# Kernel tuning notes

Hardware: AMD Instinct MI355X
Metric: run time of the kernel (lower is better)

## Reference

```python
import jax, jax.numpy as jnp
import numpy as np

B, S, IN_D, OUT_D, QD = 4, 1024, 16, 16, 32
HID, HEADS, HD, L, TED = 256, 8, 32, 4, 256
DECAY = 0.1
SCALE = HD ** -0.5


def _ln(x):
    m = x.mean(-1, keepdims=True)
    v = ((x - m) ** 2).mean(-1, keepdims=True)
    return (x - m) * jax.lax.rsqrt(v + 1e-5)


def _lin(x, w, b):
    # torch nn.Linear: y = x @ W^T + b, W is [out, in]
    return jnp.einsum('...i,oi->...o', x, w) + b


def _sin_emb(t, dim):
    half = dim // 2
    freqs = jnp.exp(-np.log(10000.0) * jnp.arange(half, dtype=jnp.float32) / (half - 1))
    a = t[:, None] * freqs[None, :]
    return jnp.concatenate([jnp.sin(a), jnp.cos(a)], axis=-1)


def _mish(x):
    return x * jnp.tanh(jax.nn.softplus(x))


def _gelu(x):
    return jax.nn.gelu(x, approximate=False)


def setup_inputs() -> dict:
    key = jax.random.key(0)
    ks = iter(jax.random.split(key, 64))

    def w(shape):
        return jax.random.normal(next(ks), shape, dtype=jnp.float32) * 0.02

    d = {}
    d['x'] = jax.random.normal(next(ks), (B, S, IN_D), dtype=jnp.float32)
    d['query'] = jax.random.normal(next(ks), (B, QD), dtype=jnp.float32)
    d['time'] = jax.random.uniform(next(ks), (B,), dtype=jnp.float32) * 1000.0
    d['tm_w1'] = w((TED * 4, TED)); d['tm_b1'] = jnp.zeros((TED * 4,), jnp.float32)
    d['tm_w2'] = w((TED, TED * 4)); d['tm_b2'] = jnp.zeros((TED,), jnp.float32)
    d['in_w'] = w((HID, IN_D)); d['in_b'] = jnp.zeros((HID,), jnp.float32)
    d['q_w1'] = w((HID, QD)); d['q_b1'] = jnp.zeros((HID,), jnp.float32)
    d['q_w2'] = w((HID, HID)); d['q_b2'] = jnp.zeros((HID,), jnp.float32)
    d['n1_w'] = jnp.ones((L, HID), jnp.float32); d['n1_b'] = jnp.zeros((L, HID), jnp.float32)
    d['qkv_w'] = w((L, 3 * HID, HID)); d['qkv_b'] = jnp.zeros((L, 3 * HID), jnp.float32)
    d['ap_w'] = w((L, HID, HID)); d['ap_b'] = jnp.zeros((L, HID), jnp.float32)
    d['rel_bias'] = w((L, 2 * S - 1, HEADS))
    d['n2_w'] = jnp.ones((L, HID), jnp.float32); d['n2_b'] = jnp.zeros((L, HID), jnp.float32)
    d['f1_w'] = w((L, 4 * HID, HID)); d['f1_b'] = jnp.zeros((L, 4 * HID), jnp.float32)
    d['f2_w'] = w((L, HID, 4 * HID)); d['f2_b'] = jnp.zeros((L, HID), jnp.float32)
    d['t1_w'] = w((L, HID, TED)); d['t1_b'] = jnp.zeros((L, HID), jnp.float32)
    d['t2_w'] = w((L, HID, HID)); d['t2_b'] = jnp.zeros((L, HID), jnp.float32)
    d['out_w'] = w((OUT_D, HID)); d['out_b'] = jnp.zeros((OUT_D,), jnp.float32)
    return d


def reference(x, query, time, tm_w1, tm_b1, tm_w2, tm_b2, in_w, in_b,
              q_w1, q_b1, q_w2, q_b2, n1_w, n1_b, qkv_w, qkv_b, ap_w, ap_b,
              rel_bias, n2_w, n2_b, f1_w, f1_b, f2_w, f2_b, t1_w, t1_b,
              t2_w, t2_b, out_w, out_b):
    Bx, Sx, _ = x.shape
    # time MLP: SinusoidalPosEmb -> Linear -> Mish -> Linear
    te = _lin(_sin_emb(time, TED), tm_w1, tm_b1)
    te = _lin(_mish(te), tm_w2, tm_b2)            # [B, TED]
    # input projection + query conditioning (relative-pos path: no abs pos emb)
    h = _lin(x, in_w, in_b)                        # [B, S, HID]
    qe = _lin(_gelu(_lin(query, q_w1, q_b1)), q_w2, q_b2)
    h = h + qe[:, None, :]
    # shared relative-distance structures
    idx = jnp.arange(Sx)
    rel = idx[:, None] - idx[None, :]              # [S, S]
    dec = jnp.exp(-DECAY * jnp.abs(rel).astype(jnp.float32))
    rel_idx = rel + S - 1                          # index into 2*max_seq_len-1 table
    for l in range(L):
        # time conditioning per block
        tp = _lin(_gelu(_lin(te, t1_w[l], t1_b[l])), t2_w[l], t2_b[l])
        xn = _ln(h + tp[:, None, :]) * n1_w[l] + n1_b[l]
        qkv = _lin(xn, qkv_w[l], qkv_b[l]).reshape(Bx, Sx, 3, HEADS, HD)
        qkv = qkv.transpose(2, 0, 3, 1, 4)          # [3, B, H, S, hd]
        q_, k_, v_ = qkv[0], qkv[1], qkv[2]
        attn = jnp.einsum('bhqd,bhkd->bhqk', q_, k_) * SCALE
        bias = rel_bias[l][rel_idx]                 # [S, S, H]
        attn = attn + (dec[:, :, None] * bias).transpose(2, 0, 1)[None]
        a = jax.nn.softmax(attn, axis=-1)
        o = jnp.einsum('bhqk,bhkd->bhqd', a, v_)
        o = o.transpose(0, 2, 1, 3).reshape(Bx, Sx, HID)
        h = h + _lin(o, ap_w[l], ap_b[l])           # residual from pre-time x
        xn2 = _ln(h) * n2_w[l] + n2_b[l]
        h = h + _lin(_gelu(_lin(xn2, f1_w[l], f1_b[l])), f2_w[l], f2_b[l])
    return _lin(h, out_w, out_b)
```

## Files before the change

kernel.cpp:

```cpp
#include <hip/hip_runtime.h>
#include <hip/hip_bf16.h>
#include <math.h>

#define S_LEN 1024
#define HID 256
#define HEADS 8
#define HD 32
#define NLAYER 4
#define TED 256
#define BATCH 4
#define DECAY 0.1f
#define ATT_SCALE 0.17677669529663687f
#define LOG2E 1.4426950408889634f

typedef __bf16 bf8_t __attribute__((ext_vector_type(8)));
typedef float f4_t __attribute__((ext_vector_type(4)));

__device__ __forceinline__ float gelu_f(float x) {
  return 0.5f * x * (1.f + erff(x * 0.70710678118654752f));
}
__device__ __forceinline__ __bf16 f2bf(float f) { return (__bf16)f; }

__global__ __launch_bounds__(256) void k_boot(
    const float* __restrict__ s0, __bf16* __restrict__ d0,
    const float* __restrict__ s1, __bf16* __restrict__ d1,
    const float* __restrict__ s2, __bf16* __restrict__ d2,
    const float* __restrict__ s3, __bf16* __restrict__ d3,
    const float* __restrict__ relb, float* __restrict__ decb_t,
    const float* __restrict__ timev,
    const float* __restrict__ tm_w1, const float* __restrict__ tm_b1,
    const float* __restrict__ query,
    const float* __restrict__ q_w1, const float* __restrict__ q_b1,
    float* __restrict__ te1, float* __restrict__ q1) {
  int bid = blockIdx.x;
  int lane = threadIdx.x & 63;
  if (bid < 1536) {
    const float* s; __bf16* d; int base;
    if (bid < 384)       { s = s0; d = d0; base = bid; }
    else if (bid < 512)  { s = s1; d = d1; base = bid - 384; }
    else if (bid < 1024) { s = s2; d = d2; base = bid - 512; }
    else                 { s = s3; d = d3; base = bid - 1024; }
    int i = (base * 256 + threadIdx.x) * 8;
    float4 a = *(const float4*)(s + i);
    float4 b = *(const float4*)(s + i + 4);
    bf8_t o;
    o[0] = f2bf(a.x); o[1] = f2bf(a.y); o[2] = f2bf(a.z); o[3] = f2bf(a.w);
    o[4] = f2bf(b.x); o[5] = f2bf(b.y); o[6] = f2bf(b.z); o[7] = f2bf(b.w);
    *(bf8_t*)(d + i) = o;
  } else if (bid < 1792) {
    int lb = bid - 1536;
    int l = lb >> 6;
    int i = (lb & 63) * 256 + threadIdx.x;
    if (i < 2047 * 8) {
      int idx = i >> 3, hh = i & 7;
      float dec = __expf(-DECAY * fabsf((float)(idx - 1023)));
      decb_t[(l * 8 + hh) * 2048 + idx] = dec * relb[(size_t)l * 2047 * 8 + i] * LOG2E;
    }
  } else if (bid < 2816) {
    int r = (bid - 1792) * 4 + (threadIdx.x >> 6);
    int o = r & 1023, b = r >> 10;
    float t = timev[b];
    float ev[4];
#pragma unroll
    for (int e = 0; e < 4; e++) {
      int k = lane * 4 + e;
      int i = k & 127;
      float f = __expf(-logf(10000.f) * (float)i / 127.f);
      float a = t * f;
      ev[e] = (k < 128) ? sinf(a) : cosf(a);
    }
    float4 w4 = *(const float4*)(tm_w1 + (size_t)o * 256 + lane * 4);
    float s = ev[0] * w4.x + ev[1] * w4.y + ev[2] * w4.z + ev[3] * w4.w;
#pragma unroll
    for (int off = 32; off; off >>= 1) s += __shfl_xor(s, off);
    if (lane == 0) {
      s += tm_b1[o];
      float sp = (s > 20.f) ? s : log1pf(__expf(s));
      te1[r] = s * tanhf(sp);
    }
  } else {
    int r = (bid - 2816) * 4 + (threadIdx.x >> 6);
    int o = r & 255, b = r >> 8;
    float s = 0.f;
    if (lane < 8) {
      float4 a4 = *(const float4*)(query + b * 32 + lane * 4);
      float4 w4 = *(const float4*)(q_w1 + (size_t)o * 32 + lane * 4);
      s = a4.x * w4.x + a4.y * w4.y + a4.z * w4.z + a4.w * w4.w;
    }
#pragma unroll
    for (int off = 32; off; off >>= 1) s += __shfl_xor(s, off);
    if (lane == 0) q1[r] = gelu_f(s + q_b1[o]);
  }
}

__global__ __launch_bounds__(256) void k_prep_b(
    const float* __restrict__ te1, const float* __restrict__ tm_w2,
    const float* __restrict__ tm_b2,
    const float* __restrict__ q1, const float* __restrict__ q_w2,
    const float* __restrict__ q_b2,
    float* __restrict__ te, float* __restrict__ qe) {
  int bid = blockIdx.x;
  int lane = threadIdx.x & 63;
  bool iste = bid < 256;
  int r = (iste ? bid : bid - 256) * 4 + (threadIdx.x >> 6);
  int o = r & 255, b = r >> 8;
  int K = iste ? 1024 : 256;
  const float* a = (iste ? te1 : q1) + (size_t)b * K;
  const float* w = (iste ? tm_w2 : q_w2) + (size_t)o * K;
  float s = 0.f;
  for (int k = lane * 4; k < K; k += 256) {
    float4 a4 = *(const float4*)(a + k);
    float4 w4 = *(const float4*)(w + k);
    s += a4.x * w4.x + a4.y * w4.y + a4.z * w4.z + a4.w * w4.w;
  }
#pragma unroll
  for (int off = 32; off; off >>= 1) s += __shfl_xor(s, off);
  if (lane == 0) {
    s += (iste ? tm_b2 : q_b2)[o];
    (iste ? te : qe)[r] = s;
  }
}

__global__ __launch_bounds__(256) void k_mid(
    const float* __restrict__ te, const float* __restrict__ t1_w,
    const float* __restrict__ t1_b, float* __restrict__ tt,
    const float* __restrict__ x, const float* __restrict__ in_w,
    const float* __restrict__ in_b, const float* __restrict__ qe,
    float* __restrict__ h) {
  int bid = blockIdx.x;
  if (bid < 1024) {
    int r = bid * 4 + (threadIdx.x >> 6);
    int lane = threadIdx.x & 63;
    int o = r & 255;
    int b = (r >> 8) & 3;
    int g = r >> 10;
    const float* a = te + (size_t)b * 256;
    const float* w = t1_w + ((size_t)(g * 256 + o)) * 256;
    float s = 0.f;
    for (int k = lane * 4; k < 256; k += 256) {
      float4 a4 = *(const float4*)(a + k);
      float4 w4 = *(const float4*)(w + k);
      s += a4.x * w4.x + a4.y * w4.y + a4.z * w4.z + a4.w * w4.w;
    }
#pragma unroll
    for (int off = 32; off; off >>= 1) s += __shfl_xor(s, off);
    if (lane == 0) tt[r] = gelu_f(s + t1_b[g * 256 + o]);
  } else {
    int row = bid - 1024;
    int b = row >> 10;
    int j = threadIdx.x;
    __shared__ float xr[16];
    if (j < 16) xr[j] = x[row * 16 + j];
    __syncthreads();
    float s = in_b[j] + qe[b * 256 + j];
    const float* w = in_w + j * 16;
#pragma unroll
    for (int i = 0; i < 16; i++) s += xr[i] * w[i];
    h[(size_t)row * 256 + j] = s;
  }
}

template <int ACT, bool APG>
__global__ __launch_bounds__(256) void k_gemv(
    const float* __restrict__ A, const float* __restrict__ W,
    const float* __restrict__ bias, float* __restrict__ out,
    int K, int OUT) {
  int r = blockIdx.x * 4 + (threadIdx.x >> 6);
  int lane = threadIdx.x & 63;
  int o = r % OUT;
  int b = (r / OUT) % BATCH;
  int g = r / (OUT * BATCH);
  const float* a = A + (size_t)((APG ? g * BATCH : 0) + b) * K;
  const float* w = W + (size_t)(g * OUT + o) * K;
  float s = 0.f;
  for (int k = lane * 4; k < K; k += 256) {
    float4 a4 = *(const float4*)(a + k);
    float4 w4 = *(const float4*)(w + k);
    s += a4.x * w4.x + a4.y * w4.y + a4.z * w4.z + a4.w * w4.w;
  }
#pragma unroll
  for (int off = 32; off; off >>= 1) s += __shfl_xor(s, off);
  if (lane == 0) {
    s += bias[g * OUT + o];
    if (ACT == 1) s = gelu_f(s);
    if (ACT == 2) {
      float sp = (s > 20.f) ? s : log1pf(__expf(s));
      s = s * tanhf(sp);
    }
    out[r] = s;
  }
}

template <int BN, int ACT, int OUTMODE, bool HASTP>
__global__ __launch_bounds__(256) void k_gemm_lnf(
    const float* __restrict__ h, const __bf16* __restrict__ W,
    const float* __restrict__ bias, void* __restrict__ Cv,
    const float* __restrict__ tp, const float* __restrict__ lw,
    const float* __restrict__ lb, int N) {
  constexpr int K = 256;
  constexpr int NJ = (BN / 2) / 16;
  constexpr int BQ = BN / 64;
  __shared__ __bf16 Al[64 * 264];
  __shared__ __bf16 Bl[2 * BN * 32];
  int tid = threadIdx.x;
  int w = tid >> 6, lane = tid & 63;
  int g = lane >> 4, c = lane & 15;
  int n0 = blockIdx.x * BN, m0 = blockIdx.y * 64;

  int srow = tid >> 2;
  int scol = (tid & 3) * 8;
  int sw = (((tid & 3) ^ ((tid >> 3) & 3))) * 8;
  const __bf16* Wb = W + (size_t)n0 * K + scol;
  bf8_t nB[2][BQ];
#pragma unroll
  for (int sub = 0; sub < 2; sub++)
#pragma unroll
    for (int q = 0; q < BQ; q++)
      nB[sub][q] = *(const bf8_t*)(Wb + (size_t)(q * 64 + srow) * K + sub * 32);

  int sub32 = tid & 31, lrow = tid >> 5;
  int colb = sub32 * 8;
  float4 lw0 = *(const float4*)(lw + colb), lw1 = *(const float4*)(lw + colb + 4);
  float4 lb0 = *(const float4*)(lb + colb), lb1 = *(const float4*)(lb + colb + 4);
  float4 tp0, tp1;
  if (HASTP) {
    const float* tpr = tp + (m0 >> 10) * 256 + colb;
    tp0 = *(const float4*)tpr; tp1 = *(const float4*)(tpr + 4);
  }
#pragma unroll
  for (int p = 0; p < 8; p++) {
    int row = p * 8 + lrow;
    const float* hr = h + (size_t)(m0 + row) * 256 + colb;
    float4 a = *(const float4*)hr;
    float4 b2 = *(const float4*)(hr + 4);
    if (HASTP) {
      a.x += tp0.x; a.y += tp0.y; a.z += tp0.z; a.w += tp0.w;
      b2.x += tp1.x; b2.y += tp1.y; b2.z += tp1.z; b2.w += tp1.w;
    }
    float sum = a.x + a.y + a.z + a.w + b2.x + b2.y + b2.z + b2.w;
    float ss = a.x * a.x + a.y * a.y + a.z * a.z + a.w * a.w +
               b2.x * b2.x + b2.y * b2.y + b2.z * b2.z + b2.w * b2.w;
#pragma unroll
    for (int m = 1; m < 32; m <<= 1) {
      sum += __shfl_xor(sum, m);
      ss += __shfl_xor(ss, m);
    }
    float mean = sum * (1.f / 256.f);
    float var = ss * (1.f / 256.f) - mean * mean;
    float rs = rsqrtf(var + 1e-5f);
    bf8_t o;
    o[0] = f2bf((a.x - mean) * rs * lw0.x + lb0.x);
    o[1] = f2bf((a.y - mean) * rs * lw0.y + lb0.y);
    o[2] = f2bf((a.z - mean) * rs * lw0.z + lb0.z);
    o[3] = f2bf((a.w - mean) * rs * lw0.w + lb0.w);
    o[4] = f2bf((b2.x - mean) * rs * lw1.x + lb1.x);
    o[5] = f2bf((b2.y - mean) * rs * lw1.y + lb1.y);
    o[6] = f2bf((b2.z - mean) * rs * lw1.z + lb1.z);
    o[7] = f2bf((b2.w - mean) * rs * lw1.w + lb1.w);
    *(bf8_t*)&Al[row * 264 + colb] = o;
  }

  int wr = (w >> 1) * 32, wc = (w & 1) * (BN / 2);
  int aseg = ((g ^ ((c >> 1) & 3))) * 8;
  f4_t acc[2][NJ];
#pragma unroll
  for (int i = 0; i < 2; i++)
#pragma unroll
    for (int j = 0; j < NJ; j++) acc[i][j] = (f4_t){0.f, 0.f, 0.f, 0.f};

#pragma unroll
  for (int ph = 0; ph < 4; ph++) {
    __syncthreads();
#pragma unroll
    for (int sub = 0; sub < 2; sub++)
#pragma unroll
      for (int q = 0; q < BQ; q++)
        *(bf8_t*)&Bl[sub * BN * 32 + (q * 64 + srow) * 32 + sw] = nB[sub][q];
    __syncthreads();
    if (ph < 3) {
#pragma unroll
      for (int sub = 0; sub < 2; sub++)
#pragma unroll
        for (int q = 0; q < BQ; q++)
          nB[sub][q] = *(const bf8_t*)(Wb + (size_t)(q * 64 + srow) * K +
                                       (ph + 1) * 64 + sub * 32);
    }
#pragma unroll
    for (int sub = 0; sub < 2; sub++) {
      bf8_t af[2], bfr[NJ];
#pragma unroll
      for (int i = 0; i < 2; i++)
        af[i] = *(const bf8_t*)&Al[(wr + i * 16 + c) * 264 + ph * 64 + sub * 32 + g * 8];
#pragma unroll
      for (int j = 0; j < NJ; j++)
        bfr[j] = *(const bf8_t*)&Bl[sub * BN * 32 + (wc + j * 16 + c) * 32 + aseg];
#pragma unroll
      for (int i = 0; i < 2; i++)
#pragma unroll
        for (int j = 0; j < NJ; j++)
          acc[i][j] = __builtin_amdgcn_mfma_f32_16x16x32_bf16(af[i], bfr[j], acc[i][j], 0, 0, 0);
    }
  }
#pragma unroll
  for (int j = 0; j < NJ; j++) {
    int col = n0 + wc + j * 16 + c;
    float bv = bias[col];
#pragma unroll
    for (int i = 0; i < 2; i++) {
#pragma unroll
      for (int rr = 0; rr < 4; rr++) {
        int row = m0 + wr + i * 16 + 4 * g + rr;
        float v = acc[i][j][rr] + bv;
        if (ACT == 1) v = gelu_f(v);
        size_t idx = (size_t)row * N + col;
        if (OUTMODE == 1) ((float*)Cv)[idx] += v;
        else ((__bf16*)Cv)[idx] = f2bf(v);
      }
    }
  }
}

__global__ __launch_bounds__(256) void k_attn(
    const __bf16* __restrict__ qkv, const float* __restrict__ decb_t,
    __bf16* __restrict__ obuf) {
  __shared__ __bf16 Kl[128 * 40];
  __shared__ __bf16 Vt[32 * 136];
  __shared__ __bf16 Pl[4][16 * 136];
  __shared__ float db[1088];

  int tid = threadIdx.x;
  int w = tid >> 6, lane = tid & 63;
  int g = lane >> 4, c = lane & 15;
  int bh = blockIdx.y;
  int b = bh >> 3, hh = bh & 7;
  int q0 = blockIdx.x * 64;

  for (int i = tid; i < 1087; i += 256) db[i] = decb_t[hh * 2048 + q0 + i];

  bf8_t qraw = *(const bf8_t*)(qkv + ((size_t)(b * S_LEN + q0 + w * 16 + c)) * 768 + hh * 32 + 8 * g);
  bf8_t qfrag;
#pragma unroll
  for (int i = 0; i < 8; i++) qfrag[i] = f2bf((float)qraw[i] * (ATT_SCALE * LOG2E));

  float ps_acc[4] = {0.f, 0.f, 0.f, 0.f};
  f4_t o0 = {0.f, 0.f, 0.f, 0.f}, o1 = {0.f, 0.f, 0.f, 0.f};

  int rowb = w * 16 + 4 * g;
  __bf16* Plw = &Pl[w][0];

  int kvr = tid & 127;
  int part = tid >> 7;
  const __bf16* base0 = qkv + ((size_t)(b * S_LEN + kvr)) * 768 + hh * 32 + part * 16;
  bf8_t k8a = *(const bf8_t*)(base0 + 256);
  bf8_t k8b = *(const bf8_t*)(base0 + 264);
  bf8_t v8a = *(const bf8_t*)(base0 + 512);
  bf8_t v8b = *(const bf8_t*)(base0 + 520);

  for (int c0 = 0; c0 < S_LEN; c0 += 128) {
    __syncthreads();
    {
      *(bf8_t*)&Kl[kvr * 40 + part * 16] = k8a;
      *(bf8_t*)&Kl[kvr * 40 + part * 16 + 8] = k8b;
      int d0s = part * 16;
#pragma unroll
      for (int jj = 0; jj < 8; jj++) Vt[(d0s + jj) * 136 + kvr] = v8a[jj];
#pragma unroll
      for (int jj = 0; jj < 8; jj++) Vt[(d0s + 8 + jj) * 136 + kvr] = v8b[jj];
    }
    __syncthreads();
    if (c0 + 128 < S_LEN) {
      const __bf16* basen = base0 + (size_t)(c0 + 128) * 768;
      k8a = *(const bf8_t*)(basen + 256);
      k8b = *(const bf8_t*)(basen + 264);
      v8a = *(const bf8_t*)(basen + 512);
      v8b = *(const bf8_t*)(basen + 520);
    }

    f4_t sc[8];
    f4_t zero4 = {0.f, 0.f, 0.f, 0.f};
    __builtin_amdgcn_s_setprio(1);
#pragma unroll
    for (int j = 0; j < 8; j++) {
      bf8_t kfrag = *(const bf8_t*)&Kl[(j * 16 + c) * 40 + g * 8];
      sc[j] = __builtin_amdgcn_mfma_f32_16x16x32_bf16(qfrag, kfrag, zero4, 0, 0, 0);
    }
    __builtin_amdgcn_s_setprio(0);
#pragma unroll
    for (int j = 0; j < 8; j++) {
      int bidx = rowb + 1023 - (c0 + j * 16 + c);
#pragma unroll
      for (int r = 0; r < 4; r++) {
        float p = exp2f(sc[j][r] + db[bidx + r]);
        ps_acc[r] += p;
        Plw[(4 * g + r) * 136 + j * 16 + c] = f2bf(p);
      }
    }
    __builtin_amdgcn_s_setprio(1);
#pragma unroll
    for (int ss = 0; ss < 4; ss++) {
      bf8_t pa = *(const bf8_t*)&Plw[c * 136 + ss * 32 + g * 8];
      bf8_t v0 = *(const bf8_t*)&Vt[c * 136 + ss * 32 + g * 8];
      bf8_t v1 = *(const bf8_t*)&Vt[(c + 16) * 136 + ss * 32 + g * 8];
      o0 = __builtin_amdgcn_mfma_f32_16x16x32_bf16(pa, v0, o0, 0, 0, 0);
      o1 = __builtin_amdgcn_mfma_f32_16x16x32_bf16(pa, v1, o1, 0, 0, 0);
    }
    __builtin_amdgcn_s_setprio(0);
  }

#pragma unroll
  for (int r = 0; r < 4; r++) {
#pragma unroll
    for (int m = 1; m < 16; m <<= 1) ps_acc[r] += __shfl_xor(ps_acc[r], m);
    float inv = 1.f / ps_acc[r];
    size_t rowg = (size_t)(b * S_LEN + q0 + rowb + r);
    obuf[rowg * 256 + hh * 32 + c] = f2bf(o0[r] * inv);
    obuf[rowg * 256 + hh * 32 + 16 + c] = f2bf(o1[r] * inv);
  }
}

__global__ __launch_bounds__(512) void k_back(
    const __bf16* __restrict__ obb, float* __restrict__ h,
    const __bf16* __restrict__ wap, const float* __restrict__ apb,
    const float* __restrict__ n2w, const float* __restrict__ n2b,
    const __bf16* __restrict__ wf1, const float* __restrict__ f1b,
    const __bf16* __restrict__ wf2, const float* __restrict__ f2b) {
  __shared__ __bf16 Asm[16 * 264];
  __shared__ __bf16 Bl[2 * 256 * 32];
  __shared__ __bf16 y1l[16 * 1032];
  __shared__ float red[16][8][2];

  int tid = threadIdx.x;
  int w = tid >> 6, lane = tid & 63;
  int g = lane >> 4, c = lane & 15;
  int m0 = blockIdx.x * 16;
  int srow = tid >> 2;
  int scol = (tid & 3) * 8;
  int sw = (((tid & 3) ^ ((srow >> 1) & 3))) * 8;
  int wc = w * 32;
  int axor = (c >> 1) & 3;
  int boff0 = (wc + c) * 32 + ((g ^ axor)) * 8;
  int boff1 = (wc + 16 + c) * 32 + ((g ^ axor)) * 8;
  int col0 = wc + c, col1 = wc + 16 + c;
  f4_t zero4 = {0.f, 0.f, 0.f, 0.f};

  bf8_t nB[2][2];
  auto prefetch = [&](const __bf16* base, int K, int ko) {
#pragma unroll
    for (int s = 0; s < 2; s++)
#pragma unroll
      for (int q = 0; q < 2; q++)
        nB[s][q] = *(const bf8_t*)(base + (size_t)(q * 128 + srow) * K + ko + s * 32 + scol);
  };
  auto stageB = [&]() {
    __syncthreads();
#pragma unroll
    for (int s = 0; s < 2; s++)
#pragma unroll
      for (int q = 0; q < 2; q++)
        *(bf8_t*)&Bl[s * 8192 + (q * 128 + srow) * 32 + sw] = nB[s][q];
    __syncthreads();
  };
  f4_t a0, a1;
  auto mstep = [&](const __bf16* Ab, int AS, int ko) {
#pragma unroll
    for (int s = 0; s < 2; s++) {
      bf8_t af = *(const bf8_t*)&Ab[c * AS + ko + s * 32 + g * 8];
      bf8_t b0 = *(const bf8_t*)&Bl[s * 8192 + boff0];
      bf8_t b1 = *(const bf8_t*)&Bl[s * 8192 + boff1];
      a0 = __builtin_amdgcn_mfma_f32_16x16x32_bf16(af, b0, a0, 0, 0, 0);
      a1 = __builtin_amdgcn_mfma_f32_16x16x32_bf16(af, b1, a1, 0, 0, 0);
    }
  };

  prefetch(wap, 256, 0);
  {
    int row = tid >> 5, gr = tid & 31;
    *(bf8_t*)&Asm[row * 264 + gr * 8] = *(const bf8_t*)(obb + (size_t)(m0 + row) * 256 + gr * 8);
  }

  a0 = zero4; a1 = zero4;
#pragma unroll
  for (int ph = 0; ph < 4; ph++) {
    stageB();
    if (ph < 3) prefetch(wap, 256, (ph + 1) * 64);
    else prefetch(wf1, 256, 0);
    mstep(Asm, 264, ph * 64);
  }

  float hn[2][4];
  {
    float b0v = apb[col0], b1v = apb[col1];
    float ps[4], pq[4];
#pragma unroll
    for (int r = 0; r < 4; r++) {
      size_t row = (size_t)(m0 + 4 * g + r);
      float v0 = a0[r] + b0v + h[row * 256 + col0];
      float v1 = a1[r] + b1v + h[row * 256 + col1];
      h[row * 256 + col0] = v0;
      h[row * 256 + col1] = v1;
      hn[0][r] = v0; hn[1][r] = v1;
      ps[r] = v0 + v1;
      pq[r] = v0 * v0 + v1 * v1;
    }
#pragma unroll
    for (int r = 0; r < 4; r++) {
#pragma unroll
      for (int m = 1; m < 16; m <<= 1) {
        ps[r] += __shfl_xor(ps[r], m);
        pq[r] += __shfl_xor(pq[r], m);
      }
    }
    if (c == 0) {
#pragma unroll
      for (int r = 0; r < 4; r++) {
        red[4 * g + r][w][0] = ps[r];
        red[4 * g + r][w][1] = pq[r];
      }
    }
  }
  __syncthreads();
  {
    float n2w0 = n2w[col0], n2b0 = n2b[col0];
    float n2w1 = n2w[col1], n2b1 = n2b[col1];
#pragma unroll
    for (int r = 0; r < 4; r++) {
      int row = 4 * g + r;
      float S = 0.f, Q = 0.f;
#pragma unroll
      for (int ww = 0; ww < 8; ww++) { S += red[row][ww][0]; Q += red[row][ww][1]; }
      float mean = S * (1.f / 256.f);
      float var = Q * (1.f / 256.f) - mean * mean;
      float rs = rsqrtf(var + 1e-5f);
      Asm[row * 264 + col0] = f2bf((hn[0][r] - mean) * rs * n2w0 + n2b0);
      Asm[row * 264 + col1] = f2bf((hn[1][r] - mean) * rs * n2w1 + n2b1);
    }
  }

#pragma unroll
  for (int nc = 0; nc < 4; nc++) {
    a0 = zero4; a1 = zero4;
#pragma unroll
    for (int ph = 0; ph < 4; ph++) {
      stageB();
      if (ph < 3) prefetch(wf1 + nc * 65536, 256, (ph + 1) * 64);
      else if (nc < 3) prefetch(wf1 + (nc + 1) * 65536, 256, 0);
      else prefetch(wf2, 1024, 0);
      mstep(Asm, 264, ph * 64);
    }
    float b0v = f1b[nc * 256 + col0], b1v = f1b[nc * 256 + col1];
#pragma unroll
    for (int r = 0; r < 4; r++) {
      y1l[(4 * g + r) * 1032 + nc * 256 + col0] = f2bf(gelu_f(a0[r] + b0v));
      y1l[(4 * g + r) * 1032 + nc * 256 + col1] = f2bf(gelu_f(a1[r] + b1v));
    }
  }

  a0 = zero4; a1 = zero4;
#pragma unroll
  for (int ph = 0; ph < 16; ph++) {
    stageB();
    if (ph < 15) prefetch(wf2, 1024, (ph + 1) * 64);
    mstep(y1l, 1032, ph * 64);
  }
  {
    float b0v = f2b[col0], b1v = f2b[col1];
#pragma unroll
    for (int r = 0; r < 4; r++) {
      size_t row = (size_t)(m0 + 4 * g + r);
      h[row * 256 + col0] += a0[r] + b0v;
      h[row * 256 + col1] += a1[r] + b1v;
    }
  }
}

__global__ __launch_bounds__(256) void k_out(
    const float* __restrict__ hbuf, const float* __restrict__ out_w,
    const float* __restrict__ out_b, float* __restrict__ out) {
  int tid = threadIdx.x;
  int r = blockIdx.x * 16 + (tid >> 4);
  int c = tid & 15;
  const float4* hr = (const float4*)(hbuf + (size_t)r * 256);
  const float4* w4 = (const float4*)(out_w + c * 256);
  float s = out_b[c];
#pragma unroll 8
  for (int k = 0; k < 64; k++) {
    float4 a = hr[k], b = w4[k];
    s += a.x * b.x + a.y * b.y + a.z * b.z + a.w * b.w;
  }
  out[r * 16 + c] = s;
}

extern "C" void kernel_launch(void* const* d_in, const int* in_sizes, int n_in,
                              void* d_out, int out_size, void* d_ws, size_t ws_size,
                              hipStream_t stream) {
  const float* x      = (const float*)d_in[0];
  const float* query  = (const float*)d_in[1];
  const float* timev  = (const float*)d_in[2];
  const float* tm_w1  = (const float*)d_in[3];
  const float* tm_b1  = (const float*)d_in[4];
  const float* tm_w2  = (const float*)d_in[5];
  const float* tm_b2  = (const float*)d_in[6];
  const float* in_w   = (const float*)d_in[7];
  const float* in_b   = (const float*)d_in[8];
  const float* q_w1   = (const float*)d_in[9];
  const float* q_b1   = (const float*)d_in[10];
  const float* q_w2   = (const float*)d_in[11];
  const float* q_b2   = (const float*)d_in[12];
  const float* n1_w   = (const float*)d_in[13];
  const float* n1_b   = (const float*)d_in[14];
  const float* qkv_w  = (const float*)d_in[15];
  const float* qkv_b  = (const float*)d_in[16];
  const float* ap_w   = (const float*)d_in[17];
  const float* ap_b   = (const float*)d_in[18];
  const float* relb   = (const float*)d_in[19];
  const float* n2_w   = (const float*)d_in[20];
  const float* n2_b   = (const float*)d_in[21];
  const float* f1_w   = (const float*)d_in[22];
  const float* f1_b   = (const float*)d_in[23];
  const float* f2_w   = (const float*)d_in[24];
  const float* f2_b   = (const float*)d_in[25];
  const float* t1_w   = (const float*)d_in[26];
  const float* t1_b   = (const float*)d_in[27];
  const float* t2_w   = (const float*)d_in[28];
  const float* t2_b   = (const float*)d_in[29];
  const float* out_w  = (const float*)d_in[30];
  const float* out_b  = (const float*)d_in[31];
  float* out = (float*)d_out;

  float* ws = (float*)d_ws;
  float*  h    = ws;
  __bf16* qkvb = (__bf16*)(ws + 1572864);
  __bf16* obb  = (__bf16*)(ws + 3145728);
  __bf16* wqkv = (__bf16*)(ws + 5767168);
  __bf16* wap  = (__bf16*)(ws + 6160384);
  __bf16* wf1  = (__bf16*)(ws + 6291456);
  __bf16* wf2  = (__bf16*)(ws + 6815744);
  float* decb  = ws + 7340032;
  float* qe    = decb + 65536;
  float* tp    = qe + 1024;
  float* te1   = tp + 4096;
  float* te    = te1 + 4096;
  float* q1    = te + 1024;
  float* tt    = q1 + 1024;

  k_boot<<<3072, 256, 0, stream>>>(qkv_w, wqkv, ap_w, wap, f1_w, wf1, f2_w, wf2,
                                   relb, decb, timev, tm_w1, tm_b1,
                                   query, q_w1, q_b1, te1, q1);
  k_prep_b<<<512, 256, 0, stream>>>(te1, tm_w2, tm_b2, q1, q_w2, q_b2, te, qe);
  k_mid<<<5120, 256, 0, stream>>>(te, t1_w, t1_b, tt, x, in_w, in_b, qe, h);
  k_gemv<0, true><<<1024, 256, 0, stream>>>(tt, t2_w, t2_b, tp, 256, 256);

  for (int l = 0; l < NLAYER; l++) {
    k_gemm_lnf<128, 0, 2, true><<<dim3(6, 64), 256, 0, stream>>>(
        h, wqkv + (size_t)l * 196608, qkv_b + l * 768, qkvb,
        tp + l * 1024, n1_w + l * 256, n1_b + l * 256, 768);
    k_attn<<<dim3(16, 32), 256, 0, stream>>>(qkvb, decb + l * 16384, obb);
    k_back<<<256, 512, 0, stream>>>(
        obb, h, wap + (size_t)l * 65536, ap_b + l * 256,
        n2_w + l * 256, n2_b + l * 256,
        wf1 + (size_t)l * 262144, f1_b + l * 1024,
        wf2 + (size_t)l * 262144, f2_b + l * 256);
  }
  k_out<<<256, 256, 0, stream>>>(h, out_w, out_b, out);
}
```

Before: 279.8 us.

## Fuse next-layer LN+QKV projection and output projection into k_back epilogue

The back-half kernel (attn proj + FFN) now keeps the updated residual rows in registers and directly computes the next layer's time-shifted LayerNorm and QKV projection, writing the bf16 qkv buffer. On the last layer it instead computes the final output projection from shared memory. This removes the separate QKV GEMM and output kernels for most layers, cutting launches and a reread of h. The cost is that each 16-row block does the QKV GEMM with only 256 blocks, which may underuse the GPU compared with the 384-block dedicated GEMM, and shared memory per block grows.

```diff
diff --git a/kernel.cpp b/kernel.cpp
--- a/kernel.cpp
+++ b/kernel.cpp
@@ -134,14 +134,9 @@
     int o = r & 255;
     int b = (r >> 8) & 3;
     int g = r >> 10;
-    const float* a = te + (size_t)b * 256;
-    const float* w = t1_w + ((size_t)(g * 256 + o)) * 256;
-    float s = 0.f;
-    for (int k = lane * 4; k < 256; k += 256) {
-      float4 a4 = *(const float4*)(a + k);
-      float4 w4 = *(const float4*)(w + k);
-      s += a4.x * w4.x + a4.y * w4.y + a4.z * w4.z + a4.w * w4.w;
-    }
+    float4 a4 = *(const float4*)(te + (size_t)b * 256 + lane * 4);
+    float4 w4 = *(const float4*)(t1_w + ((size_t)(g * 256 + o)) * 256 + lane * 4);
+    float s = a4.x * w4.x + a4.y * w4.y + a4.z * w4.z + a4.w * w4.w;
 #pragma unroll
     for (int off = 32; off; off >>= 1) s += __shfl_xor(s, off);
     if (lane == 0) tt[r] = gelu_f(s + t1_b[g * 256 + o]);
@@ -160,46 +155,27 @@
   }
 }
 
-template <int ACT, bool APG>
-__global__ __launch_bounds__(256) void k_gemv(
-    const float* __restrict__ A, const float* __restrict__ W,
-    const float* __restrict__ bias, float* __restrict__ out,
-    int K, int OUT) {
+__global__ __launch_bounds__(256) void k_t2(
+    const float* __restrict__ tt, const float* __restrict__ t2_w,
+    const float* __restrict__ t2_b, float* __restrict__ tp) {
   int r = blockIdx.x * 4 + (threadIdx.x >> 6);
   int lane = threadIdx.x & 63;
-  int o = r % OUT;
-  int b = (r / OUT) % BATCH;
-  int g = r / (OUT * BATCH);
-  const float* a = A + (size_t)((APG ? g * BATCH : 0) + b) * K;
-  const float* w = W + (size_t)(g * OUT + o) * K;
-  float s = 0.f;
-  for (int k = lane * 4; k < K; k += 256) {
-    float4 a4 = *(const float4*)(a + k);
-    float4 w4 = *(const float4*)(w + k);
-    s += a4.x * w4.x + a4.y * w4.y + a4.z * w4.z + a4.w * w4.w;
-  }
+  int o = r & 255, b = (r >> 8) & 3, g = r >> 10;
+  float4 a4 = *(const float4*)(tt + (size_t)(g * 4 + b) * 256 + lane * 4);
+  float4 w4 = *(const float4*)(t2_w + (size_t)(g * 256 + o) * 256 + lane * 4);
+  float s = a4.x * w4.x + a4.y * w4.y + a4.z * w4.z + a4.w * w4.w;
 #pragma unroll
   for (int off = 32; off; off >>= 1) s += __shfl_xor(s, off);
-  if (lane == 0) {
-    s += bias[g * OUT + o];
-    if (ACT == 1) s = gelu_f(s);
-    if (ACT == 2) {
-      float sp = (s > 20.f) ? s : log1pf(__expf(s));
-      s = s * tanhf(sp);
-    }
-    out[r] = s;
-  }
-}
-
-template <int BN, int ACT, int OUTMODE, bool HASTP>
+  if (lane == 0) tp[r] = s + t2_b[g * 256 + o];
+}
+
 __global__ __launch_bounds__(256) void k_gemm_lnf(
     const float* __restrict__ h, const __bf16* __restrict__ W,
-    const float* __restrict__ bias, void* __restrict__ Cv,
+    const float* __restrict__ bias, __bf16* __restrict__ Cv,
     const float* __restrict__ tp, const float* __restrict__ lw,
-    const float* __restrict__ lb, int N) {
-  constexpr int K = 256;
-  constexpr int NJ = (BN / 2) / 16;
-  constexpr int BQ = BN / 64;
+    const float* __restrict__ lb) {
+  constexpr int K = 256, BN = 128, NJ = 4, BQ = 2;
+  const int N = 768;
   __shared__ __bf16 Al[64 * 264];
   __shared__ __bf16 Bl[2 * BN * 32];
   int tid = threadIdx.x;
@@ -222,21 +198,16 @@
   int colb = sub32 * 8;
   float4 lw0 = *(const float4*)(lw + colb), lw1 = *(const float4*)(lw + colb + 4);
   float4 lb0 = *(const float4*)(lb + colb), lb1 = *(const float4*)(lb + colb + 4);
-  float4 tp0, tp1;
-  if (HASTP) {
-    const float* tpr = tp + (m0 >> 10) * 256 + colb;
-    tp0 = *(const float4*)tpr; tp1 = *(const float4*)(tpr + 4);
-  }
+  const float* tpr = tp + (m0 >> 10) * 256 + colb;
+  float4 tp0 = *(const float4*)tpr, tp1 = *(const float4*)(tpr + 4);
 #pragma unroll
   for (int p = 0; p < 8; p++) {
     int row = p * 8 + lrow;
     const float* hr = h + (size_t)(m0 + row) * 256 + colb;
     float4 a = *(const float4*)hr;
     float4 b2 = *(const float4*)(hr + 4);
-    if (HASTP) {
-      a.x += tp0.x; a.y += tp0.y; a.z += tp0.z; a.w += tp0.w;
-      b2.x += tp1.x; b2.y += tp1.y; b2.z += tp1.z; b2.w += tp1.w;
-    }
+    a.x += tp0.x; a.y += tp0.y; a.z += tp0.z; a.w += tp0.w;
+    b2.x += tp1.x; b2.y += tp1.y; b2.z += tp1.z; b2.w += tp1.w;
     float sum = a.x + a.y + a.z + a.w + b2.x + b2.y + b2.z + b2.w;
     float ss = a.x * a.x + a.y * a.y + a.z * a.z + a.w * a.w +
                b2.x * b2.x + b2.y * b2.y + b2.z * b2.z + b2.w * b2.w;
@@ -310,11 +281,7 @@
 #pragma unroll
       for (int rr = 0; rr < 4; rr++) {
         int row = m0 + wr + i * 16 + 4 * g + rr;
-        float v = acc[i][j][rr] + bv;
-        if (ACT == 1) v = gelu_f(v);
-        size_t idx = (size_t)row * N + col;
-        if (OUTMODE == 1) ((float*)Cv)[idx] += v;
-        else ((__bf16*)Cv)[idx] = f2bf(v);
+        Cv[(size_t)row * N + col] = f2bf(acc[i][j][rr] + bv);
       }
     }
   }
@@ -418,16 +385,23 @@
   }
 }
 
+template <int NEXT>
 __global__ __launch_bounds__(512) void k_back(
     const __bf16* __restrict__ obb, float* __restrict__ h,
     const __bf16* __restrict__ wap, const float* __restrict__ apb,
     const float* __restrict__ n2w, const float* __restrict__ n2b,
     const __bf16* __restrict__ wf1, const float* __restrict__ f1b,
-    const __bf16* __restrict__ wf2, const float* __restrict__ f2b) {
-  __shared__ __bf16 Asm[16 * 264];
-  __shared__ __bf16 Bl[2 * 256 * 32];
-  __shared__ __bf16 y1l[16 * 1032];
-  __shared__ float red[16][8][2];
+    const __bf16* __restrict__ wf2, const float* __restrict__ f2b,
+    const __bf16* __restrict__ wqkvn, const float* __restrict__ qkvbn,
+    const float* __restrict__ tpn, const float* __restrict__ n1wn,
+    const float* __restrict__ n1bn, __bf16* __restrict__ qkvb,
+    const float* __restrict__ out_w, const float* __restrict__ out_b,
+    float* __restrict__ out) {
+  __shared__ __align__(16) char smem[75264];
+  __bf16* Asm = (__bf16*)smem;
+  __bf16* Bl  = (__bf16*)(smem + 8448);
+  __bf16* y1l = (__bf16*)(smem + 41216);
+  float (*red)[8][2] = (float(*)[8][2])(smem + 74240);
 
   int tid = threadIdx.x;
   int w = tid >> 6, lane = tid & 63;
@@ -477,7 +451,6 @@
     int row = tid >> 5, gr = tid & 31;
     *(bf8_t*)&Asm[row * 264 + gr * 8] = *(const bf8_t*)(obb + (size_t)(m0 + row) * 256 + gr * 8);
   }
-
   a0 = zero4; a1 = zero4;
 #pragma unroll
   for (int ph = 0; ph < 4; ph++) {
@@ -560,34 +533,112 @@
   for (int ph = 0; ph < 16; ph++) {
     stageB();
     if (ph < 15) prefetch(wf2, 1024, (ph + 1) * 64);
+    else if (NEXT == 1) prefetch(wqkvn, 256, 0);
     mstep(y1l, 1032, ph * 64);
   }
+
+  float hf[2][4];
   {
     float b0v = f2b[col0], b1v = f2b[col1];
 #pragma unroll
     for (int r = 0; r < 4; r++) {
       size_t row = (size_t)(m0 + 4 * g + r);
-      h[row * 256 + col0] += a0[r] + b0v;
-      h[row * 256 + col1] += a1[r] + b1v;
-    }
-  }
-}
-
-__global__ __launch_bounds__(256) void k_out(
-    const float* __restrict__ hbuf, const float* __restrict__ out_w,
-    const float* __restrict__ out_b, float* __restrict__ out) {
-  int tid = threadIdx.x;
-  int r = blockIdx.x * 16 + (tid >> 4);
-  int c = tid & 15;
-  const float4* hr = (const float4*)(hbuf + (size_t)r * 256);
-  const float4* w4 = (const float4*)(out_w + c * 256);
-  float s = out_b[c];
+      float v0 = h[row * 256 + col0] + a0[r] + b0v;
+      float v1 = h[row * 256 + col1] + a1[r] + b1v;
+      h[row * 256 + col0] = v0;
+      h[row * 256 + col1] = v1;
+      hf[0][r] = v0; hf[1][r] = v1;
+    }
+  }
+
+  if (NEXT == 1) {
+    int bb = m0 >> 10;
+    float t0 = tpn[bb * 256 + col0], t1 = tpn[bb * 256 + col1];
+    float v0r[4], v1r[4];
+    {
+      float ps[4], pq[4];
+#pragma unroll
+      for (int r = 0; r < 4; r++) {
+        float v0 = hf[0][r] + t0, v1 = hf[1][r] + t1;
+        v0r[r] = v0; v1r[r] = v1;
+        ps[r] = v0 + v1;
+        pq[r] = v0 * v0 + v1 * v1;
+      }
+#pragma unroll
+      for (int r = 0; r < 4; r++) {
+#pragma unroll
+        for (int m = 1; m < 16; m <<= 1) {
+          ps[r] += __shfl_xor(ps[r], m);
+          pq[r] += __shfl_xor(pq[r], m);
+        }
+      }
+      __syncthreads();
+      if (c == 0) {
+#pragma unroll
+        for (int r = 0; r < 4; r++) {
+          red[4 * g + r][w][0] = ps[r];
+          red[4 * g + r][w][1] = pq[r];
+        }
+      }
+    }
+    __syncthreads();
+    {
+      float w0 = n1wn[col0], b0 = n1bn[col0];
+      float w1 = n1wn[col1], b1 = n1bn[col1];
+#pragma unroll
+      for (int r = 0; r < 4; r++) {
+        int row = 4 * g + r;
+        float S = 0.f, Q = 0.f;
+#pragma unroll
+        for (int ww = 0; ww < 8; ww++) { S += red[row][ww][0]; Q += red[row][ww][1]; }
+        float mean = S * (1.f / 256.f);
+        float var = Q * (1.f / 256.f) - mean * mean;
+        float rs = rsqrtf(var + 1e-5f);
+        Asm[row * 264 + col0] = f2bf((v0r[r] - mean) * rs * w0 + b0);
+        Asm[row * 264 + col1] = f2bf((v1r[r] - mean) * rs * w1 + b1);
+      }
+    }
+#pragma unroll
+    for (int nc = 0; nc < 3; nc++) {
+      a0 = zero4; a1 = zero4;
+#pragma unroll
+      for (int ph = 0; ph < 4; ph++) {
+        stageB();
+        if (ph < 3) prefetch(wqkvn + nc * 65536, 256, (ph + 1) * 64);
+        else if (nc < 2) prefetch(wqkvn + (nc + 1) * 65536, 256, 0);
+        mstep(Asm, 264, ph * 64);
+      }
+      float b0v = qkvbn[nc * 256 + col0], b1v = qkvbn[nc * 256 + col1];
+#pragma unroll
+      for (int r = 0; r < 4; r++) {
+        size_t row = (size_t)(m0 + 4 * g + r);
+        qkvb[row * 768 + nc * 256 + col0] = f2bf(a0[r] + b0v);
+        qkvb[row * 768 + nc * 256 + col1] = f2bf(a1[r] + b1v);
+      }
+    }
+  } else if (NEXT == 2) {
+    float* hl = (float*)(smem + 8448);
+    __syncthreads();
+#pragma unroll
+    for (int r = 0; r < 4; r++) {
+      int row = 4 * g + r;
+      hl[row * 260 + col0] = hf[0][r];
+      hl[row * 260 + col1] = hf[1][r];
+    }
+    __syncthreads();
+    if (tid < 256) {
+      int r = tid >> 4, cc = tid & 15;
+      const float4* hr = (const float4*)&hl[r * 260];
+      const float4* w4 = (const float4*)(out_w + cc * 256);
+      float s = out_b[cc];
 #pragma unroll 8
-  for (int k = 0; k < 64; k++) {
-    float4 a = hr[k], b = w4[k];
-    s += a.x * b.x + a.y * b.y + a.z * b.z + a.w * b.w;
-  }
-  out[r * 16 + c] = s;
+      for (int k = 0; k < 64; k++) {
+        float4 a = hr[k], b = w4[k];
+        s += a.x * b.x + a.y * b.y + a.z * b.z + a.w * b.w;
+      }
+      out[(m0 + r) * 16 + cc] = s;
+    }
+  }
 }
 
 extern "C" void kernel_launch(void* const* d_in, const int* in_sizes, int n_in,
@@ -648,18 +699,30 @@
                                    query, q_w1, q_b1, te1, q1);
   k_prep_b<<<512, 256, 0, stream>>>(te1, tm_w2, tm_b2, q1, q_w2, q_b2, te, qe);
   k_mid<<<5120, 256, 0, stream>>>(te, t1_w, t1_b, tt, x, in_w, in_b, qe, h);
-  k_gemv<0, true><<<1024, 256, 0, stream>>>(tt, t2_w, t2_b, tp, 256, 256);
+  k_t2<<<1024, 256, 0, stream>>>(tt, t2_w, t2_b, tp);
+
+  k_gemm_lnf<<<dim3(6, 64), 256, 0, stream>>>(
+      h, wqkv, qkv_b, qkvb, tp, n1_w, n1_b);
 
   for (int l = 0; l < NLAYER; l++) {
-    k_gemm_lnf<128, 0, 2, true><<<dim3(6, 64), 256, 0, stream>>>(
-        h, wqkv + (size_t)l * 196608, qkv_b + l * 768, qkvb,
-        tp + l * 1024, n1_w + l * 256, n1_b + l * 256, 768);
     k_attn<<<dim3(16, 32), 256, 0, stream>>>(qkvb, decb + l * 16384, obb);
-    k_back<<<256, 512, 0, stream>>>(
-        obb, h, wap + (size_t)l * 65536, ap_b + l * 256,
-        n2_w + l * 256, n2_b + l * 256,
-        wf1 + (size_t)l * 262144, f1_b + l * 1024,
-        wf2 + (size_t)l * 262144, f2_b + l * 256);
-  }
-  k_out<<<256, 256, 0, stream>>>(h, out_w, out_b, out);
-}
+    if (l < NLAYER - 1) {
+      k_back<1><<<256, 512, 0, stream>>>(
+          obb, h, wap + (size_t)l * 65536, ap_b + l * 256,
+          n2_w + l * 256, n2_b + l * 256,
+          wf1 + (size_t)l * 262144, f1_b + l * 1024,
+          wf2 + (size_t)l * 262144, f2_b + l * 256,
+          wqkv + (size_t)(l + 1) * 196608, qkv_b + (l + 1) * 768,
+          tp + (l + 1) * 1024, n1_w + (l + 1) * 256, n1_b + (l + 1) * 256, qkvb,
+          nullptr, nullptr, nullptr);
+    } else {
+      k_back<2><<<256, 512, 0, stream>>>(
+          obb, h, wap + (size_t)l * 65536, ap_b + l * 256,
+          n2_w + l * 256, n2_b + l * 256,
+          wf1 + (size_t)l * 262144, f1_b + l * 1024,
+          wf2 + (size_t)l * 262144, f2_b + l * 256,
+          nullptr, nullptr, nullptr, nullptr, nullptr, nullptr,
+          out_w, out_b, out);
+    }
+  }
+}
```

Measured after the change: 280.9 us. About the same (+0.4%).
